# Optimization experiments

Hardware: AMD Instinct MI355X
Metric: run time of the kernel (lower is better)

## Reference

```python
import jax, jax.numpy as jnp
import numpy as np

# Standard VVC 8-tap luma interpolation filter (16 fractional phases), /256 as in source
_LUMA = np.array([
    [0, 0, 0, 64, 0, 0, 0, 0],
    [0, 1, -3, 63, 4, -2, 1, 0],
    [-1, 2, -5, 62, 8, -3, 1, 0],
    [-1, 3, -8, 60, 13, -4, 1, 0],
    [-1, 4, -10, 58, 17, -5, 1, 0],
    [-1, 4, -11, 52, 26, -8, 3, -1],
    [-1, 3, -9, 47, 31, -10, 4, -1],
    [-1, 4, -11, 45, 34, -10, 4, -1],
    [-1, 4, -11, 40, 40, -11, 4, -1],
    [-1, 4, -10, 34, 45, -11, 4, -1],
    [-1, 4, -10, 31, 47, -9, 3, -1],
    [-1, 3, -8, 26, 52, -11, 4, -1],
    [0, 1, -5, 17, 58, -10, 4, -1],
    [0, 1, -4, 13, 60, -8, 3, -1],
    [0, 1, -3, 8, 62, -5, 2, -1],
    [0, 1, -2, 4, 63, -3, 1, 0]], dtype=np.float32) / 256.0

TAPS = 8          # filter_length for standard luma
LOG2_NORM = 12    # final normalization 2**12


def _phase_tables(out_len, in_len, scale):
    """Static (trace-time) per-output-position tap indices and fractional phase,
    replicating the source exactly: ref = int(i*16384/scale); integer = ref>>4; frac = ref&15;
    tap index = clamp(integer + k - TAPS//2 + 1, 0, in_len-1)."""
    refs = np.array([int(i * 16384 / scale) for i in range(out_len)], dtype=np.int64)
    integer = refs >> 4
    frac = refs & 15
    idx = np.clip(integer[:, None] + np.arange(TAPS)[None, :] - TAPS // 2 + 1, 0, in_len - 1)
    return jnp.asarray(idx, jnp.int32), jnp.asarray(frac, jnp.int32)


def _upsample(x, filt, scale):
    B, C, H, W = x.shape
    new_W, new_H = int(W * scale), int(H * scale)

    # Horizontal pass: per-output-column phase-dependent 8-tap MAC
    idx_w, frac_w = _phase_tables(new_W, W, scale)
    coef_w = filt[frac_w]                      # [new_W, TAPS]
    x_h = jnp.zeros((B, C, H, new_W), x.dtype)
    for k in range(TAPS):                      # small fixed tap loop, vectorized over B,C,H,new_W
        x_h = x_h + coef_w[:, k] * x[:, :, :, idx_w[:, k]]

    # Vertical pass: per-output-row phase-dependent 8-tap MAC
    idx_h, frac_h = _phase_tables(new_H, H, scale)
    coef_h = filt[frac_h]                      # [new_H, TAPS]
    x_v = jnp.zeros((B, C, new_H, new_W), x.dtype)
    for k in range(TAPS):
        x_v = x_v + coef_h[:, k][:, None] * x_h[:, :, idx_h[:, k], :]

    return x_v / (2 ** LOG2_NORM)


def setup_inputs() -> dict:
    key = jax.random.key(0)
    x = jax.random.normal(key, (2, 8, 540, 960), dtype=jnp.float32)
    return {"x": x, "luma_filter": jnp.asarray(_LUMA), "scale_factor": 3}


def reference(x, luma_filter, scale_factor):
    return _upsample(x, luma_filter, scale_factor)
```

## Files before the change

### kernel.cpp

```cpp
#include <hip/hip_runtime.h>

#define Hh 540
#define Ww 960
#define OHh 1620
#define OWw 2880
#define OW4 720

typedef float floatx4 __attribute__((ext_vector_type(4)));

__global__ __launch_bounds__(256) void vtm_upsample(
    const float* __restrict__ x,
    const float* __restrict__ filt,
    const int* __restrict__ scale_p,
    float* __restrict__ out)
{
    __shared__ float s_f[16][8];
    __shared__ float s_sum[16];
    const int tid = threadIdx.x;
    if (tid < 128) ((float*)s_f)[tid] = filt[tid];
    __syncthreads();
    if (tid < 16) {
        float s = 0.f;
        #pragma unroll
        for (int k = 0; k < 8; ++k) s += s_f[tid][k];
        s_sum[tid] = s;
    }
    __syncthreads();

    const unsigned scale = (unsigned)*scale_p;
    const unsigned oy = blockIdx.x;
    const unsigned bc = blockIdx.y;
    const float inv = 1.0f / 4096.0f;

    const float* __restrict__ xp = x + (size_t)bc * (Hh * Ww);
    float* __restrict__ op = out + (size_t)bc * ((size_t)OHh * OWw) + (size_t)oy * OWw;

    const unsigned refy = (oy * 16384u) / scale;
    const int iy = (int)(refy >> 4);
    const int fy = (int)(refy & 15u);
    const int r0 = min(max(iy - 3, 0), Hh - 1);
    const int r7 = min(max(iy + 4, 0), Hh - 1);
    const bool rsat = (r0 == r7);
    const float Shi = s_sum[fy] * inv;

    for (unsigned g = (unsigned)tid; g < OW4; g += 256u) {
        float vals[4];
        int cc[4], ff[4];
        bool cs[4];
        #pragma unroll
        for (int u = 0; u < 4; ++u) {
            const unsigned ox = 4u * g + (unsigned)u;
            const unsigned refx = (ox * 16384u) / scale;
            const int ix = (int)(refx >> 4);
            ff[u] = (int)(refx & 15u);
            const int c0 = min(max(ix - 3, 0), Ww - 1);
            const int c7 = min(max(ix + 4, 0), Ww - 1);
            cc[u] = c0;
            cs[u] = (c0 == c7);
        }

        if (rsat) {
            const float* __restrict__ rp = xp + r0 * Ww;
            #pragma unroll
            for (int u = 0; u < 4; ++u) {
                if (cs[u]) {
                    vals[u] = rp[cc[u]] * s_sum[ff[u]] * Shi;
                } else {
                    const unsigned ox = 4u * g + (unsigned)u;
                    const int ix = (int)(((ox * 16384u) / scale) >> 4);
                    float h = 0.f;
                    #pragma unroll
                    for (int k = 0; k < 8; ++k) {
                        const int cx = min(max(ix + k - 3, 0), Ww - 1);
                        h = fmaf(s_f[ff[u]][k], rp[cx], h);
                    }
                    vals[u] = h * Shi;
                }
            }
        } else {
            #pragma unroll
            for (int u = 0; u < 4; ++u) {
                const unsigned ox = 4u * g + (unsigned)u;
                const int ix = (int)(((ox * 16384u) / scale) >> 4);
                float acc = 0.f;
                #pragma unroll
                for (int j = 0; j < 8; ++j) {
                    const int ry = min(max(iy + j - 3, 0), Hh - 1);
                    const float* __restrict__ rp2 = xp + ry * Ww;
                    float h = 0.f;
                    #pragma unroll
                    for (int k = 0; k < 8; ++k) {
                        const int cx = min(max(ix + k - 3, 0), Ww - 1);
                        h = fmaf(s_f[ff[u]][k], rp2[cx], h);
                    }
                    acc = fmaf(s_f[fy][j], h, acc);
                }
                vals[u] = acc * inv;
            }
        }

        floatx4 r4 = { vals[0], vals[1], vals[2], vals[3] };
        __builtin_nontemporal_store(r4, reinterpret_cast<floatx4*>(op + 4u * g));
    }
}

extern "C" void kernel_launch(void* const* d_in, const int* in_sizes, int n_in,
                              void* d_out, int out_size, void* d_ws, size_t ws_size,
                              hipStream_t stream) {
    const float* x       = (const float*)d_in[0];
    const float* filt    = (const float*)d_in[1];
    const int*   scale_p = (const int*)d_in[2];
    float* out = (float*)d_out;
    dim3 grid(OHh, 16), block(256);
    vtm_upsample<<<grid, block, 0, stream>>>(x, filt, scale_p, out);
}
```

Baseline: 382.7 us.

## Process 30 output rows per block and reuse the saturated-row horizontal filter

Each block now covers 30 consecutive output rows instead of one, with per-row vertical phase data precomputed into shared memory. The horizontal filter result for the clamped last input row is computed once per thread and reused for every saturated output row, so those rows need only a scale and a store. Non-saturated rows still do the full 8x8 filter. It assumes saturated rows form a suffix of each block's rows, and it switches from nontemporal stores to regular stores.

```diff
diff --git a/kernel.cpp b/kernel.cpp
--- a/kernel.cpp
+++ b/kernel.cpp
@@ -5,18 +5,24 @@
 #define OHh 1620
 #define OWw 2880
 #define OW4 720
+#define RPB 30
 
 typedef float floatx4 __attribute__((ext_vector_type(4)));
 
 __global__ __launch_bounds__(256) void vtm_upsample(
-    const float* __restrict__ x,
-    const float* __restrict__ filt,
-    const int* __restrict__ scale_p,
-    float* __restrict__ out)
+    const float* __restrict__ x, const float* __restrict__ filt,
+    const int* __restrict__ scale_p, float* __restrict__ out)
 {
     __shared__ float s_f[16][8];
     __shared__ float s_sum[16];
+    __shared__ float s_wy[RPB];
+    __shared__ unsigned s_rm[RPB];
+
     const int tid = threadIdx.x;
+    const unsigned scale = (unsigned)*scale_p;
+    const float inv = 1.0f / 4096.0f;
+    const unsigned oy0 = blockIdx.y * RPB;
+
     if (tid < 128) ((float*)s_f)[tid] = filt[tid];
     __syncthreads();
     if (tid < 16) {
@@ -26,81 +32,86 @@
         s_sum[tid] = s;
     }
     __syncthreads();
+    if (tid < RPB) {
+        const unsigned oy = oy0 + (unsigned)tid;
+        const unsigned ref = (oy * 16384u) / scale;
+        const int ii = (int)(ref >> 4);
+        const unsigned f = ref & 15u;
+        const int lo = min(max(ii - 3, 0), Hh - 1);
+        const int hi = min(max(ii + 4, 0), Hh - 1);
+        s_rm[tid] = (unsigned)lo | (f << 10) | ((lo == hi) ? 0x4000u : 0u)
+                  | ((unsigned)(min(max(ii, -8), 4095) + 8) << 15);
+        s_wy[tid] = s_sum[f] * inv;
+    }
+    __syncthreads();
 
-    const unsigned scale = (unsigned)*scale_p;
-    const unsigned oy = blockIdx.x;
-    const unsigned bc = blockIdx.y;
-    const float inv = 1.0f / 4096.0f;
+    const unsigned bc = blockIdx.z;
+    const float* __restrict__ xp = x + (size_t)bc * (Hh * Ww);
+    float* __restrict__ op = out + (size_t)bc * ((size_t)OHh * OWw);
+    const unsigned g = blockIdx.x * 256u + (unsigned)tid;
+    if (g >= OW4) return;
 
-    const float* __restrict__ xp = x + (size_t)bc * (Hh * Ww);
-    float* __restrict__ op = out + (size_t)bc * ((size_t)OHh * OWw) + (size_t)oy * OWw;
-
-    const unsigned refy = (oy * 16384u) / scale;
-    const int iy = (int)(refy >> 4);
-    const int fy = (int)(refy & 15u);
-    const int r0 = min(max(iy - 3, 0), Hh - 1);
-    const int r7 = min(max(iy + 4, 0), Hh - 1);
-    const bool rsat = (r0 == r7);
-    const float Shi = s_sum[fy] * inv;
-
-    for (unsigned g = (unsigned)tid; g < OW4; g += 256u) {
-        float vals[4];
-        int cc[4], ff[4];
-        bool cs[4];
+    float vx[4];
+    int   ixs[4], fxs[4];
+    {
+        const float* __restrict__ rp = xp + (Hh - 1) * Ww;
         #pragma unroll
         for (int u = 0; u < 4; ++u) {
             const unsigned ox = 4u * g + (unsigned)u;
             const unsigned refx = (ox * 16384u) / scale;
             const int ix = (int)(refx >> 4);
-            ff[u] = (int)(refx & 15u);
+            const int fx = (int)(refx & 15u);
+            ixs[u] = ix; fxs[u] = fx;
             const int c0 = min(max(ix - 3, 0), Ww - 1);
             const int c7 = min(max(ix + 4, 0), Ww - 1);
-            cc[u] = c0;
-            cs[u] = (c0 == c7);
-        }
-
-        if (rsat) {
-            const float* __restrict__ rp = xp + r0 * Ww;
-            #pragma unroll
-            for (int u = 0; u < 4; ++u) {
-                if (cs[u]) {
-                    vals[u] = rp[cc[u]] * s_sum[ff[u]] * Shi;
-                } else {
-                    const unsigned ox = 4u * g + (unsigned)u;
-                    const int ix = (int)(((ox * 16384u) / scale) >> 4);
-                    float h = 0.f;
-                    #pragma unroll
-                    for (int k = 0; k < 8; ++k) {
-                        const int cx = min(max(ix + k - 3, 0), Ww - 1);
-                        h = fmaf(s_f[ff[u]][k], rp[cx], h);
-                    }
-                    vals[u] = h * Shi;
+            if (c0 == c7) {
+                vx[u] = rp[c0] * s_sum[fx];
+            } else {
+                float h = 0.f;
+                #pragma unroll
+                for (int k = 0; k < 8; ++k) {
+                    const int cx = min(max(ix + k - 3, 0), Ww - 1);
+                    h = fmaf(s_f[fx][k], rp[cx], h);
                 }
-            }
-        } else {
-            #pragma unroll
-            for (int u = 0; u < 4; ++u) {
-                const unsigned ox = 4u * g + (unsigned)u;
-                const int ix = (int)(((ox * 16384u) / scale) >> 4);
-                float acc = 0.f;
-                #pragma unroll
-                for (int j = 0; j < 8; ++j) {
-                    const int ry = min(max(iy + j - 3, 0), Hh - 1);
-                    const float* __restrict__ rp2 = xp + ry * Ww;
-                    float h = 0.f;
-                    #pragma unroll
-                    for (int k = 0; k < 8; ++k) {
-                        const int cx = min(max(ix + k - 3, 0), Ww - 1);
-                        h = fmaf(s_f[ff[u]][k], rp2[cx], h);
-                    }
-                    acc = fmaf(s_f[fy][j], h, acc);
-                }
-                vals[u] = acc * inv;
+                vx[u] = h;
             }
         }
+    }
 
-        floatx4 r4 = { vals[0], vals[1], vals[2], vals[3] };
-        __builtin_nontemporal_store(r4, reinterpret_cast<floatx4*>(op + 4u * g));
+    float* o0 = op + (size_t)oy0 * OWw + 4u * g;
+
+    int rs = 0;
+    while (rs < RPB && !(s_rm[rs] & 0x4000u)) ++rs;
+    for (int r = 0; r < rs; ++r) {
+        const unsigned rm = s_rm[r];
+        const int fy = (int)((rm >> 10) & 15u);
+        const int iy = (int)((rm >> 15) & 8191u) - 8;
+        float vals[4];
+        #pragma unroll
+        for (int u = 0; u < 4; ++u) {
+            float acc = 0.f;
+            #pragma unroll
+            for (int j = 0; j < 8; ++j) {
+                const int ry = min(max(iy + j - 3, 0), Hh - 1);
+                const float* __restrict__ rp2 = xp + ry * Ww;
+                float h = 0.f;
+                #pragma unroll
+                for (int k = 0; k < 8; ++k) {
+                    const int cx = min(max(ixs[u] + k - 3, 0), Ww - 1);
+                    h = fmaf(s_f[fxs[u]][k], rp2[cx], h);
+                }
+                acc = fmaf(s_f[fy][j], h, acc);
+            }
+            vals[u] = acc * inv;
+        }
+        floatx4 v = { vals[0], vals[1], vals[2], vals[3] };
+        *reinterpret_cast<floatx4*>(o0 + (size_t)r * OWw) = v;
+    }
+
+    for (int r = rs; r < RPB; ++r) {
+        const float wy = s_wy[r];
+        floatx4 v = { vx[0] * wy, vx[1] * wy, vx[2] * wy, vx[3] * wy };
+        *reinterpret_cast<floatx4*>(o0 + (size_t)r * OWw) = v;
     }
 }
 
@@ -111,6 +122,6 @@
     const float* filt    = (const float*)d_in[1];
     const int*   scale_p = (const int*)d_in[2];
     float* out = (float*)d_out;
-    dim3 grid(OHh, 16), block(256);
+    dim3 grid(3, OHh / RPB, 16), block(256);
     vtm_upsample<<<grid, block, 0, stream>>>(x, filt, scale_p, out);
 }
```

Result: faster. 319.7 us (-16.5%).
